# Kernel optimization log

Hardware: AMD Instinct MI355X
Metric: run time of the kernel (lower is better)

Reference implementation:

```python
import jax, jax.numpy as jnp
import numpy as np
import math

N, LQ, D, H, L, P, DFF, NL = 16, 300, 256, 8, 3, 4, 1024, 6
TLENS = (4096, 2048, 1024)
T = sum(TLENS)
TEMP = 10000.0

def _ln(x, g, b, eps=1e-5):
    m = x.mean(-1, keepdims=True)
    v = ((x - m) ** 2).mean(-1, keepdims=True)
    return (x - m) * jax.lax.rsqrt(v + eps) * g + b

def _mlp2(x, w0, b0, w1, b1):
    return jax.nn.relu(x @ w0.T + b0) @ w1.T + b1

def _sine_embed(ref):
    # ref: (N, LQ, 2) (center, width) -> (N, LQ, 2*D)
    dim_t = TEMP ** (2.0 * (jnp.arange(D) // 2) / D)
    p = ref * (2.0 * math.pi)
    def inter(v):
        return jnp.stack([jnp.sin(v[..., 0::2]), jnp.cos(v[..., 1::2])], -1).reshape(v.shape[:-1] + (-1,))
    pc = p[..., 0:1] / dim_t
    pw = p[..., 1:2] / dim_t
    return jnp.concatenate([inter(pc), inter(pw)], -1)

def _mha(q, k, v, in_w, in_b, out_w, out_b):
    Nb, Lq, Dm = q.shape
    Dh = Dm // H
    wq, wk, wv = jnp.split(in_w, 3, 0)
    bq, bk, bv = jnp.split(in_b, 3, 0)
    qh = (q @ wq.T + bq).reshape(Nb, Lq, H, Dh)
    kh = (k @ wk.T + bk).reshape(Nb, Lq, H, Dh)
    vh = (v @ wv.T + bv).reshape(Nb, Lq, H, Dh)
    att = jax.nn.softmax(jnp.einsum('nqhd,nkhd->nhqk', qh, kh) / math.sqrt(Dh), -1)
    o = jnp.einsum('nhqk,nkhd->nqhd', att, vh).reshape(Nb, Lq, Dm)
    return o @ out_w.T + out_b

def _deform_attn(q, ref, src, pad_mask, t_lens, start, ow, ob, aww, awb, vw, vb, pw, pb):
    # q: (N,LQ,D); ref: (N,LQ,L,2) normalized (center,width); src: (N,T,D)
    Nb, Lq, Dm = q.shape
    Dh = Dm // H
    val = (src @ vw.T + vb) * (~pad_mask)[..., None]
    val = val.reshape(Nb, -1, H, Dh).transpose(0, 2, 1, 3)  # (N,H,T,Dh)
    off = (q @ ow.T + ob).reshape(Nb, Lq, H, L, P)
    aw = jax.nn.softmax((q @ aww.T + awb).reshape(Nb, Lq, H, L * P), -1).reshape(Nb, Lq, H, L, P)
    # 1-D deformable sampling locations: center + offset/P * width * 0.5
    loc = ref[:, :, None, :, 0, None] + off / P * ref[:, :, None, :, 1, None] * 0.5  # (N,LQ,H,L,P)
    tl = t_lens[None, None, None, :, None]
    x = loc * tl.astype(loc.dtype) - 0.5  # align_corners=False linear sampling
    x0f = jnp.floor(x)
    f = x - x0f
    x0 = x0f.astype(jnp.int32)
    m0 = (x0 >= 0) & (x0 < tl)
    m1 = (x0 + 1 >= 0) & (x0 + 1 < tl)
    st = start[None, None, None, :, None]
    i0 = st + jnp.clip(x0, 0, tl - 1)
    i1 = st + jnp.clip(x0 + 1, 0, tl - 1)
    def tr(a):
        return a.transpose(0, 2, 1, 3, 4).reshape(Nb, H, Lq * L * P)
    g0 = jnp.take_along_axis(val, tr(i0)[..., None], axis=2)  # (N,H,M,Dh)
    g1 = jnp.take_along_axis(val, tr(i1)[..., None], axis=2)
    samp = g0 * ((1.0 - tr(f)) * tr(m0))[..., None] + g1 * (tr(f) * tr(m1))[..., None]
    samp = samp.reshape(Nb, H, Lq, L * P, Dh)
    w = tr(aw).reshape(Nb, H, Lq, L * P)
    o = jnp.einsum('nhqk,nhqkd->nqhd', w, samp).reshape(Nb, Lq, Dm)
    return o @ pw.T + pb

def _forward(tgt, enc_output_segments, feature_durations, src, src_valid_ratios,
             grid_w0, grid_b0, grid_w1, grid_b1, qs_w0, qs_b0, qs_w1, qs_b1,
             sa_in_w, sa_in_b, sa_out_w, sa_out_b,
             n1_g, n1_b, n2_g, n2_b, n3_g, n3_b,
             off_w, off_b, aw_w, aw_b, val_w, val_b, outp_w, outp_b,
             ffn_w1, ffn_b1, ffn_w2, ffn_b2,
             temporal_lens, level_start_index, src_padding_mask):
    seg = jax.lax.stop_gradient(enc_output_segments)  # original detaches proposals
    ref = jnp.stack([seg[..., 0], jnp.exp(seg[..., 1])], -1)  # (N,LQ,2) center,width
    out = tgt
    for l in range(NL):
        ref_in = (ref / feature_durations[:, None, None])[:, :, None, :] * src_valid_ratios[:, None, :, None]
        sine = _sine_embed(ref)
        raw_qpos = _mlp2(sine, grid_w0, grid_b0, grid_w1, grid_b1)
        qpos = _mlp2(out, qs_w0, qs_b0, qs_w1, qs_b1) * raw_qpos
        q = out + qpos
        out = _ln(out + _mha(q, q, out, sa_in_w[l], sa_in_b[l], sa_out_w[l], sa_out_b[l]), n1_g[l], n1_b[l])
        ca = _deform_attn(out + qpos, ref_in, src, src_padding_mask, temporal_lens, level_start_index,
                          off_w[l], off_b[l], aw_w[l], aw_b[l], val_w[l], val_b[l], outp_w[l], outp_b[l])
        out = _ln(out + ca, n2_g[l], n2_b[l])
        ff = jax.nn.relu(out @ ffn_w1[l].T + ffn_b1[l]) @ ffn_w2[l].T + ffn_b2[l]
        out = _ln(out + ff, n3_g[l], n3_b[l])
    return out

def setup_inputs():
    key = jax.random.key(0)
    ks = iter(jax.random.split(key, 64))
    def nrm(shape, s=0.02):
        return (s * jax.random.normal(next(ks), shape)).astype(jnp.float32)
    dur = 64.0
    inp = {}
    inp['tgt'] = nrm((N, LQ, D), 1.0)
    c = jax.random.uniform(next(ks), (N, LQ)) * dur
    w = jnp.log(jax.random.uniform(next(ks), (N, LQ)) * 4.0 + 0.5)
    inp['enc_output_segments'] = jnp.stack([c, w], -1)
    inp['feature_durations'] = jnp.full((N,), dur, jnp.float32)
    inp['src'] = nrm((N, T, D), 1.0)
    inp['temporal_lens'] = jnp.array(TLENS, jnp.int32)
    inp['level_start_index'] = jnp.array(np.cumsum((0,) + TLENS[:-1]), jnp.int32)
    inp['src_valid_ratios'] = jnp.ones((N, L), jnp.float32)
    inp['src_padding_mask'] = jnp.zeros((N, T), bool)
    inp['grid_w0'] = nrm((D, 2 * D)); inp['grid_b0'] = jnp.zeros((D,))
    inp['grid_w1'] = nrm((D, D)); inp['grid_b1'] = jnp.zeros((D,))
    inp['qs_w0'] = nrm((D, D)); inp['qs_b0'] = jnp.zeros((D,))
    inp['qs_w1'] = nrm((D, D)); inp['qs_b1'] = jnp.zeros((D,))
    inp['sa_in_w'] = nrm((NL, 3 * D, D)); inp['sa_in_b'] = jnp.zeros((NL, 3 * D))
    inp['sa_out_w'] = nrm((NL, D, D)); inp['sa_out_b'] = jnp.zeros((NL, D))
    for nm in ('n1', 'n2', 'n3'):
        inp[nm + '_g'] = jnp.ones((NL, D)); inp[nm + '_b'] = jnp.zeros((NL, D))
    inp['off_w'] = nrm((NL, H * L * P, D))
    inp['off_b'] = (jax.random.uniform(next(ks), (NL, H * L * P)) * 2.0 - 1.0) * P
    inp['aw_w'] = nrm((NL, H * L * P, D)); inp['aw_b'] = jnp.zeros((NL, H * L * P))
    inp['val_w'] = nrm((NL, D, D)); inp['val_b'] = jnp.zeros((NL, D))
    inp['outp_w'] = nrm((NL, D, D)); inp['outp_b'] = jnp.zeros((NL, D))
    inp['ffn_w1'] = nrm((NL, DFF, D)); inp['ffn_b1'] = jnp.zeros((NL, DFF))
    inp['ffn_w2'] = nrm((NL, D, DFF)); inp['ffn_b2'] = jnp.zeros((NL, D))
    return inp

def reference(tgt, enc_output_segments, feature_durations, src, temporal_lens, level_start_index,
              src_valid_ratios, src_padding_mask,
              grid_w0, grid_b0, grid_w1, grid_b1, qs_w0, qs_b0, qs_w1, qs_b1,
              sa_in_w, sa_in_b, sa_out_w, sa_out_b,
              n1_g, n1_b, n2_g, n2_b, n3_g, n3_b,
              off_w, off_b, aw_w, aw_b, val_w, val_b, outp_w, outp_b,
              ffn_w1, ffn_b1, ffn_w2, ffn_b2):
    return _forward(tgt, enc_output_segments, feature_durations, src, src_valid_ratios,
                    grid_w0, grid_b0, grid_w1, grid_b1, qs_w0, qs_b0, qs_w1, qs_b1,
                    sa_in_w, sa_in_b, sa_out_w, sa_out_b,
                    n1_g, n1_b, n2_g, n2_b, n3_g, n3_b,
                    off_w, off_b, aw_w, aw_b, val_w, val_b, outp_w, outp_b,
                    ffn_w1, ffn_b1, ffn_w2, ffn_b2,
                    temporal_lens, level_start_index, src_padding_mask)
```

## Files before the change

### kernel.cpp

```cpp
#include <hip/hip_runtime.h>
#include <cstdint>

#define NB   16
#define LQN  300
#define DM   256
#define NH   8
#define DH   32
#define NLV  3
#define DFFN 1024
#define NLAY 6
#define TT   7168
#define MROW (NB*LQN)
#define SROW (NB*TT)

typedef __attribute__((ext_vector_type(8))) short bf16x8;
typedef __attribute__((ext_vector_type(4))) float f32x4;

__device__ __forceinline__ float bf2f(short u) {
  unsigned x = ((unsigned)(unsigned short)u) << 16;
  return __builtin_bit_cast(float, x);
}
__device__ __forceinline__ short f2bf(float f) {
  unsigned u = __builtin_bit_cast(unsigned, f);
  u += 0x7fffu + ((u >> 16) & 1u);
  return (short)(u >> 16);
}
__device__ __forceinline__ void load_lds16(const void* g, void* l) {
  __builtin_amdgcn_global_load_lds(
      (const __attribute__((address_space(1))) unsigned int*)g,
      (__attribute__((address_space(3))) unsigned int*)l, 16, 0, 0);
}
#define MFMA(a,b,c) __builtin_amdgcn_mfma_f32_16x16x32_bf16((a),(b),(c),0,0,0)

struct CvtPtrs { const float* p[12]; };

__global__ __launch_bounds__(256)
void cvt_all_kernel(CvtPtrs ptrs, short* __restrict__ dst)
{
  const long gid = (long)blockIdx.x*256 + threadIdx.x;
  const long cums[13] = {0,32768,49152,65536,81920,376832,475136,512000,
                         548864,647168,745472,1138688,1531904};
  int s = 0;
  #pragma unroll
  for (int i = 1; i < 12; ++i) s += (gid >= cums[i]) ? 1 : 0;
  const long rel = gid - cums[s];
  const float4 v = ((const float4*)ptrs.p[s])[rel];
  long dstIdx = gid;
  if (s == 6) { const long l = rel/6144, w = rel%6144; dstIdx = 475136 + l*12288 + w; }
  else if (s == 7) { const long l = rel/6144, w = rel%6144; dstIdx = 475136 + l*12288 + 6144 + w; }
  ((short4*)dst)[dstIdx] = make_short4(f2bf(v.x), f2bf(v.y), f2bf(v.z), f2bf(v.w));
}

#define VLS 264

__global__ __launch_bounds__(512, 1)
void val_gemm(const float* __restrict__ src, const short* __restrict__ Bw,
              const float* __restrict__ bias, short* __restrict__ Cb,
              const unsigned char* __restrict__ rowmask)
{
  __shared__ short Bs[256*VLS];
  const int tid = threadIdx.x, wid = tid >> 6, lane = tid & 63;
  const int fr = lane & 15, fq = lane >> 4;

  for (int t = tid; t < 8192; t += 512) {
    const int row = t >> 5, ch = t & 31;
    const bf16x8 v = *(const bf16x8*)(Bw + row*256 + ch*8);
    *(bf16x8*)&Bs[row*VLS + ch*8] = v;
  }
  __syncthreads();

  const int rbase = (blockIdx.x*8 + wid) * 16;

  f32x4 acc[16] = {};
  bf16x8 aA, aB;

  auto loadA = [&](bf16x8& a, int ks) {
    const float* ap = src + (long)(rbase + fr)*256 + ks*32 + fq*8;
    const float4 f0 = *(const float4*)ap;
    const float4 f1 = *(const float4*)(ap + 4);
    bf16x8 t;
    t[0]=f2bf(f0.x); t[1]=f2bf(f0.y); t[2]=f2bf(f0.z); t[3]=f2bf(f0.w);
    t[4]=f2bf(f1.x); t[5]=f2bf(f1.y); t[6]=f2bf(f1.z); t[7]=f2bf(f1.w);
    a = t;
  };

  loadA(aA, 0);
  #pragma unroll
  for (int ks = 0; ks < 8; ++ks) {
    if (ks + 1 < 8) { if ((ks & 1) == 0) loadA(aB, ks + 1); else loadA(aA, ks + 1); }
    const bf16x8 a = ((ks & 1) == 0) ? aA : aB;
    #pragma unroll
    for (int nt = 0; nt < 16; ++nt) {
      const bf16x8 b = *(const bf16x8*)&Bs[(nt*16 + fr)*VLS + ks*32 + fq*8];
      acc[nt] = MFMA(a, b, acc[nt]);
    }
  }

  #pragma unroll
  for (int r = 0; r < 4; ++r) {
    const int grow = rbase + fq*4 + r;
    const float msc = rowmask[grow] ? 0.0f : 1.0f;
    #pragma unroll
    for (int nt = 0; nt < 16; ++nt) {
      const int gcol = nt*16 + fr;
      Cb[(long)grow*256 + gcol] = f2bf((acc[nt][r] + bias[gcol]) * msc);
    }
  }
}

template<int EPI>
__global__ __launch_bounds__(256)
void gemm64(const short* __restrict__ A, const short* __restrict__ B,
            const float* __restrict__ bias, const float* __restrict__ bias2,
            float* __restrict__ Cf, short* __restrict__ Cb, short* __restrict__ Cb2,
            int M, int N, int K, int ldc,
            const float* __restrict__ rawq, const float* __restrict__ resid)
{
  __shared__ short As[2][64*64];
  __shared__ short Bs[2][64*64];
  const int tid = threadIdx.x, wid = tid >> 6, lane = tid & 63;
  const int wr = wid >> 1, wc = wid & 1;
  const int fr = lane & 15, fq = lane >> 4;
  const int bm = blockIdx.x, bn = blockIdx.y;
  const int lrow = lane >> 3;
  const int schk = ((lane & 7) ^ lrow) * 8;
  const int nk = K >> 6;

  f32x4 acc[2][2] = {};

  auto stg = [&](int kt, int bsel) {
    const int k0 = kt << 6;
    #pragma unroll
    for (int i = 0; i < 2; ++i) {
      const int rr = wid*16 + i*8 + lrow;
      load_lds16(A + (long)(bm*64 + rr)*K + k0 + schk, &As[bsel][(wid*16 + i*8)*64]);
      load_lds16(B + (long)(bn*64 + rr)*K + k0 + schk, &Bs[bsel][(wid*16 + i*8)*64]);
    }
  };

  stg(0, 0);
  for (int t = 0; t < nk; ++t) {
    const int cur = t & 1;
    if (t + 1 < nk) {
      stg(t + 1, cur ^ 1);
      asm volatile("s_waitcnt vmcnt(4)" ::: "memory");
    } else {
      asm volatile("s_waitcnt vmcnt(0)" ::: "memory");
    }
    __builtin_amdgcn_s_barrier();
    __builtin_amdgcn_sched_barrier(0);
    #pragma unroll
    for (int kk = 0; kk < 64; kk += 32) {
      bf16x8 af[2], bv[2];
      #pragma unroll
      for (int mi = 0; mi < 2; ++mi)
        af[mi] = *(const bf16x8*)&As[cur][(wr*32 + mi*16 + fr)*64 + (((kk>>3)+fq) ^ (fr&7))*8];
      #pragma unroll
      for (int ni = 0; ni < 2; ++ni)
        bv[ni] = *(const bf16x8*)&Bs[cur][(wc*32 + ni*16 + fr)*64 + (((kk>>3)+fq) ^ (fr&7))*8];
      #pragma unroll
      for (int mi = 0; mi < 2; ++mi)
        #pragma unroll
        for (int ni = 0; ni < 2; ++ni)
          acc[mi][ni] = MFMA(af[mi], bv[ni], acc[mi][ni]);
    }
    __builtin_amdgcn_s_barrier();
  }

  #pragma unroll
  for (int mi = 0; mi < 2; ++mi) {
    #pragma unroll
    for (int r = 0; r < 4; ++r) {
      const int grow = bm*64 + wr*32 + mi*16 + fq*4 + r;
      #pragma unroll
      for (int ni = 0; ni < 2; ++ni) {
        const int gcol = bn*64 + wc*32 + ni*16 + fr;
        float v = acc[mi][ni][r];
        if (EPI == 4) v += (gcol < 96) ? bias[gcol] : bias2[gcol-96];
        else v += bias[gcol];
        const long off = (long)grow*ldc + gcol;
        if (EPI == 0) {
          if (Cf) Cf[off] = v;
          if (Cb) Cb[off] = f2bf(v);
        } else if (EPI == 1) {
          Cb[off] = f2bf(fmaxf(v, 0.0f));
        } else if (EPI == 2) {
          const float qp = v * rawq[off];
          Cf[off] = qp;
          Cb[off] = f2bf(resid[off] + qp);
        } else if (EPI == 3) {
          if (grow < MROW) { if (gcol < 512) Cb[(long)grow*512 + gcol] = f2bf(v); }
          else             { if (gcol >= 512) Cb2[(long)(grow-MROW)*256 + gcol-512] = f2bf(v); }
        } else if (EPI == 4) {
          Cf[off] = v;
        }
      }
    }
  }
}

__global__ __launch_bounds__(256)
void ew0_kernel(const float* __restrict__ tgt, float* __restrict__ out, short* __restrict__ outbf)
{
  const long i = (long)blockIdx.x*256 + threadIdx.x;
  const float4 v = ((const float4*)tgt)[i];
  ((float4*)out)[i] = v;
  ((short4*)outbf)[i] = make_short4(f2bf(v.x), f2bf(v.y), f2bf(v.z), f2bf(v.w));
}

__global__ __launch_bounds__(256)
void init_ref_kernel(const float* __restrict__ seg, const float* __restrict__ dur,
                     const float* __restrict__ valid,
                     short* __restrict__ sinebf, float* __restrict__ refin)
{
  const int m = blockIdx.x;
  const int n = m / LQN;
  const int t = threadIdx.x;
  const float c = seg[(long)m*2 + 0];
  const float w = __expf(seg[(long)m*2 + 1]);
  const float e = (float)(t & ~1) * (1.0f/256.0f);
  const float invdim = __expf(-e * 9.2103403719761836f);
  const float twopi = 6.2831853071795864f;
  const float a0 = c * twopi * invdim;
  const float a1 = w * twopi * invdim;
  const float v0 = (t & 1) ? cosf(a0) : sinf(a0);
  const float v1 = (t & 1) ? cosf(a1) : sinf(a1);
  sinebf[(long)m*512 + t]       = f2bf(v0);
  sinebf[(long)m*512 + 256 + t] = f2bf(v1);
  if (t < 6) {
    const int l = t >> 1, cc = t & 1;
    const float rv = cc ? w : c;
    refin[(long)m*6 + l*2 + cc] = rv / dur[n] * valid[n*NLV + l];
  }
}

#define KPAD 320
#define KSTR 40
#define VSTR 328
#define PSTR 328

__global__ __launch_bounds__(256)
void attn_mfma(const short* __restrict__ qk, const short* __restrict__ vv,
               short* __restrict__ outb)
{
  __shared__ short Kl[KPAD*KSTR];
  __shared__ short Vt[DH*VSTR];
  __shared__ short Pl[4][16*PSTR];
  const int b = blockIdx.x;
  const int half = b & 1, h = (b >> 1) & 7, n = b >> 4;
  const int tid = threadIdx.x, wid = tid >> 6, lane = tid & 63;
  const int fr = lane & 15, fq = lane >> 4;

  const short* qkn = qk + (long)n*LQN*512;
  const short* vn  = vv + (long)n*LQN*256;

  for (int t = tid; t < KPAD*4; t += 256) {
    const int r = t >> 2, c = t & 3;
    bf16x8 kv = {}, vw = {};
    if (r < LQN) {
      kv = *(const bf16x8*)(qkn + (long)r*512 + 256 + h*32 + c*8);
      vw = *(const bf16x8*)(vn  + (long)r*256 + h*32 + c*8);
    }
    *(bf16x8*)&Kl[r*KSTR + c*8] = kv;
    #pragma unroll
    for (int j = 0; j < 8; ++j) Vt[(c*8+j)*VSTR + r] = vw[j];
  }
  for (int t = tid; t < 4*16*24; t += 256) {
    const int w = t / (16*24), rr = (t / 24) & 15, cc = t % 24;
    Pl[w][rr*PSTR + 304 + cc] = 0;
  }
  __syncthreads();

  const int tlo = half ? 10 : 0, thi = half ? 19 : 10;
  const float scl2 = 0.17677669529663687f * 1.4426950408889634f;

  for (int qt = tlo + wid; qt < thi; qt += 4) {
    const int q0 = qt * 16;
    const int qrow = min(q0 + fr, LQN-1);
    const bf16x8 qf = *(const bf16x8*)(qkn + (long)qrow*512 + h*32 + fq*8);
    f32x4 s[19];
    #pragma unroll
    for (int t = 0; t < 19; ++t) {
      const bf16x8 kf = *(const bf16x8*)&Kl[(t*16+fr)*KSTR + fq*8];
      s[t] = MFMA(qf, kf, ((f32x4){0.f,0.f,0.f,0.f}));
    }
    float mx[4] = {-3e38f,-3e38f,-3e38f,-3e38f};
    #pragma unroll
    for (int t = 0; t < 19; ++t) {
      const bool valid = (t < 18) || (fr < 12);
      #pragma unroll
      for (int r = 0; r < 4; ++r) if (valid) mx[r] = fmaxf(mx[r], s[t][r]);
    }
    #pragma unroll
    for (int r = 0; r < 4; ++r) {
      #pragma unroll
      for (int o = 1; o < 16; o <<= 1) mx[r] = fmaxf(mx[r], __shfl_xor(mx[r], o));
      mx[r] *= scl2;
    }
    float l[4] = {0.f,0.f,0.f,0.f};
    #pragma unroll
    for (int t = 0; t < 19; ++t) {
      const bool valid = (t < 18) || (fr < 12);
      #pragma unroll
      for (int r = 0; r < 4; ++r) {
        const float p = valid ? exp2f(s[t][r]*scl2 - mx[r]) : 0.0f;
        l[r] += p;
        Pl[wid][(fq*4+r)*PSTR + t*16 + fr] = f2bf(p);
      }
    }
    #pragma unroll
    for (int r = 0; r < 4; ++r) {
      #pragma unroll
      for (int o = 1; o < 16; o <<= 1) l[r] += __shfl_xor(l[r], o);
    }
    f32x4 o0 = {}, o1 = {};
    #pragma unroll
    for (int ck = 0; ck < 10; ++ck) {
      const bf16x8 pf = *(const bf16x8*)&Pl[wid][fr*PSTR + ck*32 + fq*8];
      const bf16x8 v0 = *(const bf16x8*)&Vt[fr*VSTR + ck*32 + fq*8];
      const bf16x8 v1 = *(const bf16x8*)&Vt[(16+fr)*VSTR + ck*32 + fq*8];
      o0 = MFMA(pf, v0, o0);
      o1 = MFMA(pf, v1, o1);
    }
    #pragma unroll
    for (int r = 0; r < 4; ++r) {
      const int qq = q0 + fq*4 + r;
      if (qq < LQN) {
        const float inv = 1.0f / l[r];
        outb[((long)(n*LQN+qq))*256 + h*32 + fr]      = f2bf(o0[r]*inv);
        outb[((long)(n*LQN+qq))*256 + h*32 + 16 + fr] = f2bf(o1[r]*inv);
      }
    }
  }
}

__global__ __launch_bounds__(256)
void ln_kernel(const float* __restrict__ resid, const float* __restrict__ delta,
               const float* __restrict__ g, const float* __restrict__ b,
               float* __restrict__ of, short* __restrict__ ob,
               const float* __restrict__ qpos, short* __restrict__ caqb)
{
  const int m = blockIdx.x, c = threadIdx.x;
  const long idx = (long)m*DM + c;
  const float x = resid[idx] + delta[idx];
  float s = x, s2 = x*x;
  #pragma unroll
  for (int o = 1; o < 64; o <<= 1) { s += __shfl_xor(s, o); s2 += __shfl_xor(s2, o); }
  __shared__ float rs[4], rs2[4];
  const int w = c >> 6;
  if ((c & 63) == 0) { rs[w] = s; rs2[w] = s2; }
  __syncthreads();
  s  = rs[0]+rs[1]+rs[2]+rs[3];
  s2 = rs2[0]+rs2[1]+rs2[2]+rs2[3];
  const float mean = s * (1.0f/DM);
  const float var  = s2 * (1.0f/DM) - mean*mean;
  const float y = (x - mean) * rsqrtf(var + 1e-5f) * g[c] + b[c];
  of[idx] = y;
  if (ob) ob[idx] = f2bf(y);
  if (qpos) caqb[idx] = f2bf(y + qpos[idx]);
}

__global__ __launch_bounds__(256)
void sample_kernel(const short* __restrict__ val, int ldv,
                   const float* __restrict__ offaw, const float* __restrict__ refin,
                   const int* __restrict__ tlens, const int* __restrict__ lstart,
                   short* __restrict__ cab)
{
  const int m = blockIdx.x;
  const int n = m / LQN;
  const int tid = threadIdx.x;
  __shared__ int2  lI[96];
  __shared__ float2 lW[96];
  if ((tid & 31) == 0) {
    const int h = tid >> 5;
    const float* row = offaw + (long)m*192;
    float aw[12];
    float mx = -1e30f;
    #pragma unroll
    for (int lp = 0; lp < 12; ++lp) { aw[lp] = row[96 + h*12 + lp]; mx = fmaxf(mx, aw[lp]); }
    float sum = 0.0f;
    #pragma unroll
    for (int lp = 0; lp < 12; ++lp) { aw[lp] = __expf(aw[lp]-mx); sum += aw[lp]; }
    const float invs = 1.0f / sum;
    #pragma unroll
    for (int lp = 0; lp < 12; ++lp) {
      const int l = lp >> 2;
      const int tli = tlens[l];
      const float off = row[h*12 + lp];
      const float loc = refin[(long)m*6 + l*2] + off * 0.25f * refin[(long)m*6 + l*2 + 1] * 0.5f;
      const float x = loc * (float)tli - 0.5f;
      const float x0f = floorf(x);
      const float f = x - x0f;
      const int x0 = (int)x0f;
      const int i0 = lstart[l] + min(max(x0,   0), tli-1);
      const int i1 = lstart[l] + min(max(x0+1, 0), tli-1);
      const float wgt = aw[lp]*invs;
      const float w0 = (x0   >= 0 && x0   < tli) ? wgt*(1.0f-f) : 0.0f;
      const float w1 = (x0+1 >= 0 && x0+1 < tli) ? wgt*f        : 0.0f;
      lI[h*12 + lp] = make_int2(i0, i1);
      lW[h*12 + lp] = make_float2(w0, w1);
    }
  }
  __syncthreads();
  const int h = tid >> 5;
  const short* vb = val + (long)n*TT*ldv;
  float acc = 0.0f;
  #pragma unroll
  for (int lp = 0; lp < 12; ++lp) {
    const int e = h*12 + lp;
    const int2 ii = lI[e];
    const float2 ww = lW[e];
    acc += ww.x * bf2f(vb[(long)ii.x*ldv + tid]) + ww.y * bf2f(vb[(long)ii.y*ldv + tid]);
  }
  cab[(long)m*DM + tid] = f2bf(acc);
}

static inline void g64(hipStream_t st, int epi, const short* A, const short* B,
                       const float* bias, const float* bias2,
                       float* Cf, short* Cb, short* Cb2,
                       int M, int N, int K, int ldc,
                       const float* rawq = nullptr, const float* resid = nullptr)
{
  dim3 g(M/64, N/64), blk(256);
  switch (epi) {
    case 0: gemm64<0><<<g,blk,0,st>>>(A,B,bias,bias2,Cf,Cb,Cb2,M,N,K,ldc,rawq,resid); break;
    case 1: gemm64<1><<<g,blk,0,st>>>(A,B,bias,bias2,Cf,Cb,Cb2,M,N,K,ldc,rawq,resid); break;
    case 2: gemm64<2><<<g,blk,0,st>>>(A,B,bias,bias2,Cf,Cb,Cb2,M,N,K,ldc,rawq,resid); break;
    case 3: gemm64<3><<<g,blk,0,st>>>(A,B,bias,bias2,Cf,Cb,Cb2,M,N,K,ldc,rawq,resid); break;
    default:gemm64<4><<<g,blk,0,st>>>(A,B,bias,bias2,Cf,Cb,Cb2,M,N,K,ldc,rawq,resid); break;
  }
}

extern "C" void kernel_launch(void* const* d_in, const int* in_sizes, int n_in,
                              void* d_out, int out_size, void* d_ws, size_t ws_size,
                              hipStream_t stream)
{
  const float* tgt    = (const float*)d_in[0];
  const float* seg    = (const float*)d_in[1];
  const float* dur    = (const float*)d_in[2];
  const float* src    = (const float*)d_in[3];
  const int*   tlens  = (const int*)d_in[4];
  const int*   lstart = (const int*)d_in[5];
  const float* valid  = (const float*)d_in[6];
  const unsigned char* pmask = (const unsigned char*)d_in[7];
  const float* grid_w0 = (const float*)d_in[8];
  const float* grid_b0 = (const float*)d_in[9];
  const float* grid_w1 = (const float*)d_in[10];
  const float* grid_b1 = (const float*)d_in[11];
  const float* qs_w0 = (const float*)d_in[12];
  const float* qs_b0 = (const float*)d_in[13];
  const float* qs_w1 = (const float*)d_in[14];
  const float* qs_b1 = (const float*)d_in[15];
  const float* sa_in_w  = (const float*)d_in[16];
  const float* sa_in_b  = (const float*)d_in[17];
  const float* sa_out_w = (const float*)d_in[18];
  const float* sa_out_b = (const float*)d_in[19];
  const float* n1_g = (const float*)d_in[20];
  const float* n1_b = (const float*)d_in[21];
  const float* n2_g = (const float*)d_in[22];
  const float* n2_b = (const float*)d_in[23];
  const float* n3_g = (const float*)d_in[24];
  const float* n3_b = (const float*)d_in[25];
  const float* off_w = (const float*)d_in[26];
  const float* off_b = (const float*)d_in[27];
  const float* aw_w  = (const float*)d_in[28];
  const float* aw_b  = (const float*)d_in[29];
  const float* val_w = (const float*)d_in[30];
  const float* val_b = (const float*)d_in[31];
  const float* outp_w = (const float*)d_in[32];
  const float* outp_b = (const float*)d_in[33];
  const float* ffn_w1 = (const float*)d_in[34];
  const float* ffn_b1 = (const float*)d_in[35];
  const float* ffn_w2 = (const float*)d_in[36];
  const float* ffn_b2 = (const float*)d_in[37];

  const long W_G0=0, W_G1=131072, W_QS0=196608, W_QS1=262144, W_SAIN=327680,
             W_SAOUT=1507328, W_OFFAW=1900544, W_VAL=2195456,
             W_OUTP=2588672, W_FFN1=2981888, W_FFN2=4554752;

  char* ws = (char*)d_ws;
  short* wbf    = (short*)(ws + 0);
  short* sinebf = (short*)(ws + 70975488);
  short* ghbf   = (short*)(ws + 75890688);
  float* rawq   = (float*)(ws + 78348288);
  float* out    = (float*)(ws + 83263488);
  short* qcat   = (short*)(ws + 88178688);
  short* qbf    = qcat;
  short* outbf  = qcat + (long)MROW*DM;
  short* t1bf   = (short*)(ws + 93093888);
  float* qpos   = (float*)(ws + 95551488);
  short* qkbf   = (short*)(ws + 100466688);
  short* vbf    = (short*)(ws + 105381888);
  short* attnbf = (short*)(ws + 107839488);
  float* tmpf   = (float*)(ws + 110297088);
  short* caqb   = (short*)(ws + 115212288);
  float* offaw  = (float*)(ws + 117669888);
  short* cabf   = (short*)(ws + 128729088);
  short* ffnhbf = (short*)(ws + 131186688);
  float* refin  = (float*)(ws + 141017088);
  short* valbf  = (short*)(ws + 141132288);

  CvtPtrs cp;
  cp.p[0]=grid_w0; cp.p[1]=grid_w1; cp.p[2]=qs_w0; cp.p[3]=qs_w1; cp.p[4]=sa_in_w;
  cp.p[5]=sa_out_w; cp.p[6]=off_w; cp.p[7]=aw_w; cp.p[8]=val_w; cp.p[9]=outp_w;
  cp.p[10]=ffn_w1; cp.p[11]=ffn_w2;
  cvt_all_kernel<<<dim3(5984), dim3(256), 0, stream>>>(cp, wbf);

  ew0_kernel<<<dim3(1200), dim3(256), 0, stream>>>(tgt, out, outbf);
  init_ref_kernel<<<dim3(MROW), dim3(256), 0, stream>>>(seg, dur, valid, sinebf, refin);

  g64(stream, 1, sinebf, wbf + W_G0, grid_b0, nullptr, nullptr, ghbf, nullptr, MROW, 256, 512, 256);
  g64(stream, 0, ghbf,   wbf + W_G1, grid_b1, nullptr, rawq, nullptr, nullptr, MROW, 256, 256, 256);

  for (int l = 0; l < NLAY; ++l) {
    g64(stream, 1, outbf, wbf + W_QS0, qs_b0, nullptr, nullptr, t1bf, nullptr, MROW, 256, 256, 256);
    g64(stream, 2, t1bf,  wbf + W_QS1, qs_b1, nullptr, qpos, qbf, nullptr, MROW, 256, 256, 256,
        rawq, out);
    g64(stream, 3, qcat, wbf + W_SAIN + (long)l*196608, sa_in_b + l*768, nullptr,
        nullptr, qkbf, vbf, 2*MROW, 768, 256, 0);
    attn_mfma<<<dim3(256), dim3(256), 0, stream>>>(qkbf, vbf, attnbf);
    g64(stream, 0, attnbf, wbf + W_SAOUT + (long)l*65536, sa_out_b + l*256, nullptr,
        tmpf, nullptr, nullptr, MROW, 256, 256, 256);
    ln_kernel<<<dim3(MROW), dim3(256), 0, stream>>>(out, tmpf, n1_g + l*256, n1_b + l*256,
                                                    out, outbf, qpos, caqb);
    g64(stream, 4, caqb, wbf + W_OFFAW + (long)l*49152, off_b + l*96, aw_b + l*96,
        offaw, nullptr, nullptr, MROW, 192, 256, 192);
    val_gemm<<<dim3(896), dim3(512), 0, stream>>>(
        src, wbf + W_VAL + (long)l*65536, val_b + l*256, valbf, pmask);
    sample_kernel<<<dim3(MROW), dim3(256), 0, stream>>>(
        valbf, 256, offaw, refin, tlens, lstart, cabf);
    g64(stream, 0, cabf, wbf + W_OUTP + (long)l*65536, outp_b + l*256, nullptr,
        tmpf, nullptr, nullptr, MROW, 256, 256, 256);
    ln_kernel<<<dim3(MROW), dim3(256), 0, stream>>>(out, tmpf, n2_g + l*256, n2_b + l*256,
                                                    out, outbf, nullptr, nullptr);
    g64(stream, 1, outbf, wbf + W_FFN1 + (long)l*262144, ffn_b1 + l*1024, nullptr,
        nullptr, ffnhbf, nullptr, MROW, 1024, 256, 1024);
    g64(stream, 0, ffnhbf, wbf + W_FFN2 + (long)l*262144, ffn_b2 + l*256, nullptr,
        tmpf, nullptr, nullptr, MROW, 256, 1024, 256);
    float* of = (l == NLAY-1) ? (float*)d_out : out;
    ln_kernel<<<dim3(MROW), dim3(256), 0, stream>>>(out, tmpf, n3_g + l*256, n3_b + l*256,
                                                    of, outbf, nullptr, nullptr);
  }
}
```

Before: 1.052 ms.

## Pre-convert src to bf16 once and double rows per wave in value GEMM

The fp32 src is converted to bf16 once in the weight-conversion kernel and stored in the workspace, so each of the six per-layer value projections reads half the bytes and does no per-layer conversion. The value GEMM now handles 32 rows per wave (two 16-row tiles) and reuses each LDS B fragment for two MFMAs, halving the grid. The cost is a larger one-time conversion pass and more registers per wave, and the new workspace region must not overlap other buffers.

```diff
diff --git a/kernel.cpp b/kernel.cpp
--- a/kernel.cpp
+++ b/kernel.cpp
@@ -32,17 +32,17 @@
 }
 #define MFMA(a,b,c) __builtin_amdgcn_mfma_f32_16x16x32_bf16((a),(b),(c),0,0,0)
 
-struct CvtPtrs { const float* p[12]; };
+struct CvtPtrs { const float* p[13]; };
 
 __global__ __launch_bounds__(256)
 void cvt_all_kernel(CvtPtrs ptrs, short* __restrict__ dst)
 {
   const long gid = (long)blockIdx.x*256 + threadIdx.x;
-  const long cums[13] = {0,32768,49152,65536,81920,376832,475136,512000,
-                         548864,647168,745472,1138688,1531904};
+  const long cums[14] = {0,32768,49152,65536,81920,376832,475136,512000,
+                         548864,647168,745472,1138688,1531904,8871936};
   int s = 0;
   #pragma unroll
-  for (int i = 1; i < 12; ++i) s += (gid >= cums[i]) ? 1 : 0;
+  for (int i = 1; i < 13; ++i) s += (gid >= cums[i]) ? 1 : 0;
   const long rel = gid - cums[s];
   const float4 v = ((const float4*)ptrs.p[s])[rel];
   long dstIdx = gid;
@@ -54,7 +54,7 @@
 #define VLS 264
 
 __global__ __launch_bounds__(512, 1)
-void val_gemm(const float* __restrict__ src, const short* __restrict__ Bw,
+void val_gemm(const short* __restrict__ srcbf, const short* __restrict__ Bw,
               const float* __restrict__ bias, short* __restrict__ Cb,
               const unsigned char* __restrict__ rowmask)
 {
@@ -69,41 +69,37 @@
   }
   __syncthreads();
 
-  const int rbase = (blockIdx.x*8 + wid) * 16;
-
-  f32x4 acc[16] = {};
-  bf16x8 aA, aB;
-
-  auto loadA = [&](bf16x8& a, int ks) {
-    const float* ap = src + (long)(rbase + fr)*256 + ks*32 + fq*8;
-    const float4 f0 = *(const float4*)ap;
-    const float4 f1 = *(const float4*)(ap + 4);
-    bf16x8 t;
-    t[0]=f2bf(f0.x); t[1]=f2bf(f0.y); t[2]=f2bf(f0.z); t[3]=f2bf(f0.w);
-    t[4]=f2bf(f1.x); t[5]=f2bf(f1.y); t[6]=f2bf(f1.z); t[7]=f2bf(f1.w);
-    a = t;
-  };
-
-  loadA(aA, 0);
+  const int rbase = (blockIdx.x*8 + wid) * 32;
+
+  bf16x8 a[2][8];
+  #pragma unroll
+  for (int h = 0; h < 2; ++h)
+    #pragma unroll
+    for (int ks = 0; ks < 8; ++ks)
+      a[h][ks] = *(const bf16x8*)(srcbf + (long)(rbase + h*16 + fr)*256 + ks*32 + fq*8);
+
+  f32x4 acc[2][16] = {};
   #pragma unroll
   for (int ks = 0; ks < 8; ++ks) {
-    if (ks + 1 < 8) { if ((ks & 1) == 0) loadA(aB, ks + 1); else loadA(aA, ks + 1); }
-    const bf16x8 a = ((ks & 1) == 0) ? aA : aB;
     #pragma unroll
     for (int nt = 0; nt < 16; ++nt) {
       const bf16x8 b = *(const bf16x8*)&Bs[(nt*16 + fr)*VLS + ks*32 + fq*8];
-      acc[nt] = MFMA(a, b, acc[nt]);
-    }
-  }
-
-  #pragma unroll
-  for (int r = 0; r < 4; ++r) {
-    const int grow = rbase + fq*4 + r;
-    const float msc = rowmask[grow] ? 0.0f : 1.0f;
-    #pragma unroll
-    for (int nt = 0; nt < 16; ++nt) {
-      const int gcol = nt*16 + fr;
-      Cb[(long)grow*256 + gcol] = f2bf((acc[nt][r] + bias[gcol]) * msc);
+      acc[0][nt] = MFMA(a[0][ks], b, acc[0][nt]);
+      acc[1][nt] = MFMA(a[1][ks], b, acc[1][nt]);
+    }
+  }
+
+  #pragma unroll
+  for (int h = 0; h < 2; ++h) {
+    #pragma unroll
+    for (int r = 0; r < 4; ++r) {
+      const int grow = rbase + h*16 + fq*4 + r;
+      const float msc = rowmask[grow] ? 0.0f : 1.0f;
+      #pragma unroll
+      for (int nt = 0; nt < 16; ++nt) {
+        const int gcol = nt*16 + fr;
+        Cb[(long)grow*256 + gcol] = f2bf((acc[h][nt][r] + bias[gcol]) * msc);
+      }
     }
   }
 }
@@ -476,10 +472,11 @@
 
   const long W_G0=0, W_G1=131072, W_QS0=196608, W_QS1=262144, W_SAIN=327680,
              W_SAOUT=1507328, W_OFFAW=1900544, W_VAL=2195456,
-             W_OUTP=2588672, W_FFN1=2981888, W_FFN2=4554752;
+             W_OUTP=2588672, W_FFN1=2981888, W_FFN2=4554752, W_SRC=6127616;
 
   char* ws = (char*)d_ws;
   short* wbf    = (short*)(ws + 0);
+  short* srcbf  = wbf + W_SRC;
   short* sinebf = (short*)(ws + 70975488);
   short* ghbf   = (short*)(ws + 75890688);
   float* rawq   = (float*)(ws + 78348288);
@@ -503,8 +500,8 @@
   CvtPtrs cp;
   cp.p[0]=grid_w0; cp.p[1]=grid_w1; cp.p[2]=qs_w0; cp.p[3]=qs_w1; cp.p[4]=sa_in_w;
   cp.p[5]=sa_out_w; cp.p[6]=off_w; cp.p[7]=aw_w; cp.p[8]=val_w; cp.p[9]=outp_w;
-  cp.p[10]=ffn_w1; cp.p[11]=ffn_w2;
-  cvt_all_kernel<<<dim3(5984), dim3(256), 0, stream>>>(cp, wbf);
+  cp.p[10]=ffn_w1; cp.p[11]=ffn_w2; cp.p[12]=src;
+  cvt_all_kernel<<<dim3(34656), dim3(256), 0, stream>>>(cp, wbf);
 
   ew0_kernel<<<dim3(1200), dim3(256), 0, stream>>>(tgt, out, outbf);
   init_ref_kernel<<<dim3(MROW), dim3(256), 0, stream>>>(seg, dur, valid, sinebf, refin);
@@ -525,8 +522,8 @@
                                                     out, outbf, qpos, caqb);
     g64(stream, 4, caqb, wbf + W_OFFAW + (long)l*49152, off_b + l*96, aw_b + l*96,
         offaw, nullptr, nullptr, MROW, 192, 256, 192);
-    val_gemm<<<dim3(896), dim3(512), 0, stream>>>(
-        src, wbf + W_VAL + (long)l*65536, val_b + l*256, valbf, pmask);
+    val_gemm<<<dim3(448), dim3(512), 0, stream>>>(
+        srcbf, wbf + W_VAL + (long)l*65536, val_b + l*256, valbf, pmask);
     sample_kernel<<<dim3(MROW), dim3(256), 0, stream>>>(
         valbf, 256, offaw, refin, tlens, lstart, cabf);
     g64(stream, 0, cabf, wbf + W_OUTP + (long)l*65536, outp_b + l*256, nullptr,
```

New measurement: 1.039 ms. About the same (-1.2%).
